# Kernel tuning notes

Hardware: AMD Instinct MI355X
Metric: run time of the kernel (lower is better)

The kernel has to match this reference:

```python
import jax, jax.numpy as jnp
import numpy as np

L, N, I, H = 512, 64, 1024, 1024


def setup_inputs() -> dict:
    key = jax.random.key(0)
    ks = jax.random.split(key, 7)
    s = 0.05
    return {
        "x": jax.random.normal(ks[0], (L, N, I), dtype=jnp.float32),
        "h0": jnp.zeros((N, H), dtype=jnp.float32),
        "c0": jnp.zeros((N, H), dtype=jnp.float32),
        "W_ih": jax.random.normal(ks[1], (4 * H, I), dtype=jnp.float32) * s,
        "W_hh": jax.random.normal(ks[2], (4 * H, H), dtype=jnp.float32) * s,
        "b_ih": jax.random.normal(ks[3], (4 * H,), dtype=jnp.float32) * s,
        "b_hh": jax.random.normal(ks[4], (4 * H,), dtype=jnp.float32) * s,
        "W_out": jax.random.normal(ks[5], (I, H), dtype=jnp.float32) * s,
        "b_out": jax.random.normal(ks[6], (I,), dtype=jnp.float32) * s,
    }


def reference(x, h0, c0, W_ih, W_hh, b_ih, b_hh, W_out, b_out):
    # PyTorch LSTMCell gate order: input, forget, cell(g), output
    b = b_ih + b_hh  # fuse the two bias adds

    def step(carry, xt):
        h, c = carry
        z = xt @ W_ih.T + h @ W_hh.T + b  # [N, 4H]
        i, f, g, o = jnp.split(z, 4, axis=1)
        c = jax.nn.sigmoid(f) * c + jax.nn.sigmoid(i) * jnp.tanh(g)
        h = jax.nn.sigmoid(o) * jnp.tanh(c)
        return (h, c), None

    (h, c), _ = jax.lax.scan(step, (h0, c0), x)
    y = h @ W_out.T + b_out  # [N, I]
    return (y, h, c)
```

## Files before the change

### kernel.cpp

```cpp
#include <hip/hip_runtime.h>
#include <hip/hip_bf16.h>


#define L_STEPS 512
#define NB 64
#define HID 1024
#define GRID_LSTM 128

typedef __bf16 bf16x8 __attribute__((ext_vector_type(8)));
typedef __bf16 bf16x4 __attribute__((ext_vector_type(4)));
typedef __bf16 bf16x2 __attribute__((ext_vector_type(2)));
typedef float  f32x4  __attribute__((ext_vector_type(4)));
typedef float  f32x2  __attribute__((ext_vector_type(2)));
typedef unsigned u32x4 __attribute__((ext_vector_type(4)));

__device__ __forceinline__ float sigmoid_f(float x) {
    return 1.f / (1.f + __expf(-x));
}
__device__ __forceinline__ float tanh_f(float x) {
    return 1.f - 2.f / (1.f + __expf(2.f * x));
}

__global__ void convert_kernel(const float* __restrict__ x, const float* __restrict__ h0,
                               __bf16* __restrict__ xbf, __bf16* __restrict__ hbf,
                               unsigned* __restrict__ bar) {
    unsigned u = blockIdx.x * 256u + threadIdx.x;
    if (u < 512u) bar[u] = 0u;
    const int row = u & 63;
    const int cg  = (u >> 6) & 127;
    if (u < 8192u) {
        const float* s = h0 + (size_t)row * HID + cg * 8;
        f32x4 a = *(const f32x4*)s, b = *(const f32x4*)(s + 4);
        bf16x8 o;
        o[0]=(__bf16)a[0]; o[1]=(__bf16)a[1]; o[2]=(__bf16)a[2]; o[3]=(__bf16)a[3];
        o[4]=(__bf16)b[0]; o[5]=(__bf16)b[1]; o[6]=(__bf16)b[2]; o[7]=(__bf16)b[3];
        ((bf16x8*)hbf)[u] = o;
    }
    const int t = u >> 13;
    const float* s = x + ((size_t)t * NB + row) * HID + cg * 8;
    f32x4 a = *(const f32x4*)s, b = *(const f32x4*)(s + 4);
    bf16x8 o;
    o[0]=(__bf16)a[0]; o[1]=(__bf16)a[1]; o[2]=(__bf16)a[2]; o[3]=(__bf16)a[3];
    o[4]=(__bf16)b[0]; o[5]=(__bf16)b[1]; o[6]=(__bf16)b[2]; o[7]=(__bf16)b[3];
    ((bf16x8*)xbf)[u] = o;
}

__device__ __forceinline__ void mfma_x(const __bf16* __restrict__ act,
                                       const bf16x8 (&wfr)[2][8],
                                       f32x4 (&acc)[2][4]) {
    #pragma unroll
    for (int kk = 0; kk < 8; ++kk) {
        bf16x8 bfr[4];
        #pragma unroll
        for (int nt = 0; nt < 4; ++nt)
            bfr[nt] = *(const bf16x8*)(act + kk * 2048 + nt * 128);
        #pragma unroll
        for (int mt = 0; mt < 2; ++mt)
            #pragma unroll
            for (int nt = 0; nt < 4; ++nt)
                acc[mt][nt] = __builtin_amdgcn_mfma_f32_16x16x32_bf16(
                    wfr[mt][kk], bfr[nt], acc[mt][nt], 0, 0, 0);
    }
}

template <bool RING>
__global__ __launch_bounds__(256, 1) void lstm_kernel(
    const float* __restrict__ c0,
    const float* __restrict__ W_ih, const float* __restrict__ W_hh,
    const float* __restrict__ b_ih, const float* __restrict__ b_hh,
    const __bf16* __restrict__ xbf,
    __bf16* hbuf,
    unsigned* bar,
    float* __restrict__ out)
{
    const int tid  = threadIdx.x;
    const int lane = tid & 63;
    const int w    = tid >> 6;
    const int quad = lane >> 4;
    const int l15  = lane & 15;
    const int hbase = blockIdx.x * 8;

    __shared__ float red[4][64][44];

    bf16x8 wfx[2][8], wfh[2][8];
    #pragma unroll
    for (int mt = 0; mt < 2; ++mt) {
        const int n    = mt * 16 + l15;
        const int grow = (n >> 3) * HID + hbase + (n & 7);
        #pragma unroll
        for (int kk = 0; kk < 8; ++kk) {
            const int kcol = w * 256 + kk * 32 + quad * 8;
            {
                const float* src = W_ih + (size_t)grow * 1024 + kcol;
                f32x4 a = *(const f32x4*)src;
                f32x4 b = *(const f32x4*)(src + 4);
                bf16x8 f;
                f[0]=(__bf16)a[0]; f[1]=(__bf16)a[1]; f[2]=(__bf16)a[2]; f[3]=(__bf16)a[3];
                f[4]=(__bf16)b[0]; f[5]=(__bf16)b[1]; f[6]=(__bf16)b[2]; f[7]=(__bf16)b[3];
                wfx[mt][kk] = f;
            }
            {
                const float* src = W_hh + (size_t)grow * 1024 + kcol;
                f32x4 a = *(const f32x4*)src;
                f32x4 b = *(const f32x4*)(src + 4);
                bf16x8 f;
                f[0]=(__bf16)a[0]; f[1]=(__bf16)a[1]; f[2]=(__bf16)a[2]; f[3]=(__bf16)a[3];
                f[4]=(__bf16)b[0]; f[5]=(__bf16)b[1]; f[6]=(__bf16)b[2]; f[7]=(__bf16)b[3];
                wfh[mt][kk] = f;
            }
        }
    }

    const int p0 = tid * 2;
    const int cb = p0 >> 3;
    const int cu = p0 & 7;
    float c0v = c0[cb * HID + hbase + cu];
    float c1v = c0[cb * HID + hbase + cu + 1];

    float bias0[4], bias1[4];
    #pragma unroll
    for (int gate = 0; gate < 4; ++gate) {
        int gr = gate * HID + hbase + cu;
        bias0[gate] = b_ih[gr] + b_hh[gr];
        bias1[gate] = b_ih[gr + 1] + b_hh[gr + 1];
    }

    const int lane_off = (32 * w + quad) * 512 + l15 * 8;
    const int hstore_off = blockIdx.x * 512 + cb * 8 + cu;

    f32x4 acc[2][4];
    #pragma unroll
    for (int mt = 0; mt < 2; ++mt)
        #pragma unroll
        for (int nt = 0; nt < 4; ++nt) { f32x4 z = {0.f,0.f,0.f,0.f}; acc[mt][nt] = z; }
    mfma_x(xbf + lane_off, wfx, acc);

    const int pf0 = 128 * w + lane;
    const int pf1 = 128 * w + 64 + lane;

    for (int t = 0; t < L_STEPS; ++t) {
        for (;;) {
            unsigned f0 = __hip_atomic_load(&bar[pf0], __ATOMIC_RELAXED,
                                            __HIP_MEMORY_SCOPE_AGENT);
            unsigned f1 = __hip_atomic_load(&bar[pf1], __ATOMIC_RELAXED,
                                            __HIP_MEMORY_SCOPE_AGENT);
            if (__all((f0 >= (unsigned)t) && (f1 >= (unsigned)t))) break;
            __builtin_amdgcn_s_sleep(1);
        }

        u32x4 hb[8][4];
        const __bf16* hb_base = hbuf
            + (size_t)(RING ? t : (t & 1)) * (NB * HID) + lane_off;
        #pragma unroll
        for (int kk = 0; kk < 8; ++kk)
            #pragma unroll
            for (int nt = 0; nt < 4; ++nt) {
                const __bf16* p = hb_base + kk * 2048 + nt * 128;
                if constexpr (RING)
                    asm volatile("global_load_dwordx4 %0, %1, off"
                                 : "=v"(hb[kk][nt]) : "v"(p));
                else
                    asm volatile("global_load_dwordx4 %0, %1, off sc1"
                                 : "=v"(hb[kk][nt]) : "v"(p));
            }
        asm volatile("s_waitcnt vmcnt(16)"
            : "+v"(hb[0][0]), "+v"(hb[0][1]), "+v"(hb[0][2]), "+v"(hb[0][3]),
              "+v"(hb[1][0]), "+v"(hb[1][1]), "+v"(hb[1][2]), "+v"(hb[1][3]),
              "+v"(hb[2][0]), "+v"(hb[2][1]), "+v"(hb[2][2]), "+v"(hb[2][3]),
              "+v"(hb[3][0]), "+v"(hb[3][1]), "+v"(hb[3][2]), "+v"(hb[3][3]));
        #pragma unroll
        for (int kk = 0; kk < 4; ++kk)
            #pragma unroll
            for (int mt = 0; mt < 2; ++mt)
                #pragma unroll
                for (int nt = 0; nt < 4; ++nt)
                    acc[mt][nt] = __builtin_amdgcn_mfma_f32_16x16x32_bf16(
                        wfh[mt][kk], __builtin_bit_cast(bf16x8, hb[kk][nt]),
                        acc[mt][nt], 0, 0, 0);
        asm volatile("s_waitcnt vmcnt(0)"
            : "+v"(hb[4][0]), "+v"(hb[4][1]), "+v"(hb[4][2]), "+v"(hb[4][3]),
              "+v"(hb[5][0]), "+v"(hb[5][1]), "+v"(hb[5][2]), "+v"(hb[5][3]),
              "+v"(hb[6][0]), "+v"(hb[6][1]), "+v"(hb[6][2]), "+v"(hb[6][3]),
              "+v"(hb[7][0]), "+v"(hb[7][1]), "+v"(hb[7][2]), "+v"(hb[7][3]));
        #pragma unroll
        for (int kk = 4; kk < 8; ++kk)
            #pragma unroll
            for (int mt = 0; mt < 2; ++mt)
                #pragma unroll
                for (int nt = 0; nt < 4; ++nt)
                    acc[mt][nt] = __builtin_amdgcn_mfma_f32_16x16x32_bf16(
                        wfh[mt][kk], __builtin_bit_cast(bf16x8, hb[kk][nt]),
                        acc[mt][nt], 0, 0, 0);

        __syncthreads();

        #pragma unroll
        for (int mt = 0; mt < 2; ++mt)
            #pragma unroll
            for (int nt = 0; nt < 4; ++nt) {
                const int row0 = mt * 16 + quad * 4;
                const int col  = nt * 16 + l15;
                *(f32x4*)&red[w][col][row0] = acc[mt][nt];
            }
        __syncthreads();

        float h0v, h1v;
        {
            float z0[4], z1[4];
            #pragma unroll
            for (int gate = 0; gate < 4; ++gate) {
                const int row = gate * 8 + cu;
                f32x2 s0 = *(const f32x2*)&red[0][cb][row];
                f32x2 s1 = *(const f32x2*)&red[1][cb][row];
                f32x2 s2 = *(const f32x2*)&red[2][cb][row];
                f32x2 s3 = *(const f32x2*)&red[3][cb][row];
                z0[gate] = s0[0] + s1[0] + s2[0] + s3[0] + bias0[gate];
                z1[gate] = s0[1] + s1[1] + s2[1] + s3[1] + bias1[gate];
            }
            float ig = sigmoid_f(z0[0]), fg = sigmoid_f(z0[1]);
            float gg = tanh_f(z0[2]),    og = sigmoid_f(z0[3]);
            c0v = fg * c0v + ig * gg;
            h0v = og * tanh_f(c0v);
            ig = sigmoid_f(z1[0]); fg = sigmoid_f(z1[1]);
            gg = tanh_f(z1[2]);    og = sigmoid_f(z1[3]);
            c1v = fg * c1v + ig * gg;
            h1v = og * tanh_f(c1v);
        }

        {
            bf16x2 hv; hv[0] = (__bf16)h0v; hv[1] = (__bf16)h1v;
            unsigned hbits = __builtin_bit_cast(unsigned, hv);
            const __bf16* dst = hbuf
                + (size_t)(RING ? (t + 1) : ((t + 1) & 1)) * (NB * HID) + hstore_off;
            asm volatile("global_store_dword %0, %1, off sc1"
                         :: "v"(dst), "v"(hbits) : "memory");
        }
        if (t == L_STEPS - 1) {
            const int idx = cb * HID + hbase + cu;
            out[65536 + idx]      = h0v;
            out[65536 + idx + 1]  = h1v;
            out[131072 + idx]     = c0v;
            out[131072 + idx + 1] = c1v;
        }
        asm volatile("s_waitcnt vmcnt(0)" ::: "memory");
        if (lane == 0)
            __hip_atomic_store(&bar[blockIdx.x * 4 + w], (unsigned)(t + 1),
                               __ATOMIC_RELAXED, __HIP_MEMORY_SCOPE_AGENT);

        #pragma unroll
        for (int mt = 0; mt < 2; ++mt)
            #pragma unroll
            for (int nt = 0; nt < 4; ++nt) { f32x4 z = {0.f,0.f,0.f,0.f}; acc[mt][nt] = z; }
        if (t < L_STEPS - 1)
            mfma_x(xbf + (size_t)(t + 1) * (NB * HID) + lane_off, wfx, acc);
    }
}

__global__ void out_kernel(const float* __restrict__ base, const float* __restrict__ Wout,
                           const float* __restrict__ bout, float* __restrict__ y)
{
    const int wv   = (int)((blockIdx.x * 256u + threadIdx.x) >> 6);
    const int lane = threadIdx.x & 63;
    const int b = wv >> 10;
    const int i = wv & 1023;
    const f32x4* hp = (const f32x4*)(base + 65536 + b * HID);
    const f32x4* wp = (const f32x4*)(Wout + (size_t)i * HID);
    float acc = 0.f;
    #pragma unroll
    for (int q = 0; q < 4; ++q) {
        f32x4 hv = hp[q * 64 + lane];
        f32x4 wvv = wp[q * 64 + lane];
        acc += hv[0]*wvv[0] + hv[1]*wvv[1] + hv[2]*wvv[2] + hv[3]*wvv[3];
    }
    #pragma unroll
    for (int off = 32; off > 0; off >>= 1) acc += __shfl_down(acc, off);
    if (lane == 0) y[b * HID + i] = acc + bout[i];
}

extern "C" void kernel_launch(void* const* d_in, const int* in_sizes, int n_in,
                              void* d_out, int out_size, void* d_ws, size_t ws_size,
                              hipStream_t stream)
{
    const float* x    = (const float*)d_in[0];
    const float* h0   = (const float*)d_in[1];
    const float* c0   = (const float*)d_in[2];
    const float* W_ih = (const float*)d_in[3];
    const float* W_hh = (const float*)d_in[4];
    const float* b_ih = (const float*)d_in[5];
    const float* b_hh = (const float*)d_in[6];
    const float* Wout = (const float*)d_in[7];
    const float* bout = (const float*)d_in[8];
    float* out = (float*)d_out;

    const size_t XBF_B  = 67108864;
    const size_t RING_B = 513ull * 131072;
    const size_t need_ring = XBF_B + RING_B + 2048;
    const bool ring = ws_size >= need_ring;

    char* ws = (char*)d_ws;
    __bf16* xbf   = (__bf16*)(ws);
    __bf16* hbuf  = (__bf16*)(ws + XBF_B);
    unsigned* bar = (unsigned*)(ws + XBF_B + (ring ? RING_B : 262144));

    convert_kernel<<<16384, 256, 0, stream>>>(x, h0, xbf, hbuf, bar);
    if (ring)
        lstm_kernel<true><<<GRID_LSTM, 256, 0, stream>>>(c0, W_ih, W_hh, b_ih, b_hh,
                                                         xbf, hbuf, bar, out);
    else
        lstm_kernel<false><<<GRID_LSTM, 256, 0, stream>>>(c0, W_ih, W_hh, b_ih, b_hh,
                                                          xbf, hbuf, bar, out);
    out_kernel<<<16384, 256, 0, stream>>>(out, Wout, bout, out);
}
```

Measured before the change: 2.917 ms.

## Pipeline the LSTM step across four batch groups with per-group readiness flags

The 64-wide batch is split into four 16-column groups, each with its own readiness flag. Every block now waits only for that group's h slice, runs its recurrent MFMAs, reduces through shared memory, and one wave does the gate math and publishes that group's h. The next step's input-projection MFMAs for a group are issued before its flag is signalled. The aim is to replace the coarse whole-step spin barrier with fine-grained dataflow, so consumers can start on early groups while later ones are still in flight. In exchange there are four times as many flag polls and __syncthreads per step, and the gate math is serialized onto one wave per group.

```diff
diff --git a/kernel.cpp b/kernel.cpp
--- a/kernel.cpp
+++ b/kernel.cpp
@@ -45,21 +45,15 @@
     ((bf16x8*)xbf)[u] = o;
 }
 
-__device__ __forceinline__ void mfma_x(const __bf16* __restrict__ act,
-                                       const bf16x8 (&wfr)[2][8],
-                                       f32x4 (&acc)[2][4]) {
+__device__ __forceinline__ void mfma_x_bg(const __bf16* __restrict__ act,
+                                          const bf16x8 (&wfr)[2][8],
+                                          f32x4 (&a)[2]) {
     #pragma unroll
     for (int kk = 0; kk < 8; ++kk) {
-        bf16x8 bfr[4];
-        #pragma unroll
-        for (int nt = 0; nt < 4; ++nt)
-            bfr[nt] = *(const bf16x8*)(act + kk * 2048 + nt * 128);
+        bf16x8 b = *(const bf16x8*)(act + kk * 2048);
         #pragma unroll
         for (int mt = 0; mt < 2; ++mt)
-            #pragma unroll
-            for (int nt = 0; nt < 4; ++nt)
-                acc[mt][nt] = __builtin_amdgcn_mfma_f32_16x16x32_bf16(
-                    wfr[mt][kk], bfr[nt], acc[mt][nt], 0, 0, 0);
+            a[mt] = __builtin_amdgcn_mfma_f32_16x16x32_bf16(wfr[mt][kk], b, a[mt], 0, 0, 0);
     }
 }
 
@@ -128,131 +122,111 @@
     const int lane_off = (32 * w + quad) * 512 + l15 * 8;
     const int hstore_off = blockIdx.x * 512 + cb * 8 + cu;
 
-    f32x4 acc[2][4];
-    #pragma unroll
-    for (int mt = 0; mt < 2; ++mt)
-        #pragma unroll
-        for (int nt = 0; nt < 4; ++nt) { f32x4 z = {0.f,0.f,0.f,0.f}; acc[mt][nt] = z; }
-    mfma_x(xbf + lane_off, wfx, acc);
-
-    const int pf0 = 128 * w + lane;
-    const int pf1 = 128 * w + 64 + lane;
+    const int pfl = (32 * w + (lane & 31)) * 4;
+
+    f32x4 acc[4][2];
+    #pragma unroll
+    for (int bg = 0; bg < 4; ++bg) {
+        #pragma unroll
+        for (int mt = 0; mt < 2; ++mt) { f32x4 z = {0.f,0.f,0.f,0.f}; acc[bg][mt] = z; }
+        mfma_x_bg(xbf + lane_off + bg * 128, wfx, acc[bg]);
+    }
 
     for (int t = 0; t < L_STEPS; ++t) {
-        for (;;) {
-            unsigned f0 = __hip_atomic_load(&bar[pf0], __ATOMIC_RELAXED,
-                                            __HIP_MEMORY_SCOPE_AGENT);
-            unsigned f1 = __hip_atomic_load(&bar[pf1], __ATOMIC_RELAXED,
-                                            __HIP_MEMORY_SCOPE_AGENT);
-            if (__all((f0 >= (unsigned)t) && (f1 >= (unsigned)t))) break;
-            __builtin_amdgcn_s_sleep(1);
-        }
-
-        u32x4 hb[8][4];
-        const __bf16* hb_base = hbuf
-            + (size_t)(RING ? t : (t & 1)) * (NB * HID) + lane_off;
-        #pragma unroll
-        for (int kk = 0; kk < 8; ++kk)
-            #pragma unroll
-            for (int nt = 0; nt < 4; ++nt) {
-                const __bf16* p = hb_base + kk * 2048 + nt * 128;
+        const __bf16* hb_slot = hbuf + (size_t)(RING ? t : (t & 1)) * (NB * HID) + lane_off;
+        #pragma unroll
+        for (int bg = 0; bg < 4; ++bg) {
+            for (;;) {
+                unsigned f = __hip_atomic_load(&bar[pfl + bg], __ATOMIC_RELAXED,
+                                               __HIP_MEMORY_SCOPE_AGENT);
+                if (__all(f >= (unsigned)t)) break;
+                __builtin_amdgcn_s_sleep(1);
+            }
+
+            u32x4 hb[8];
+            #pragma unroll
+            for (int kk = 0; kk < 8; ++kk) {
+                const __bf16* p = hb_slot + bg * 128 + kk * 2048;
                 if constexpr (RING)
                     asm volatile("global_load_dwordx4 %0, %1, off"
-                                 : "=v"(hb[kk][nt]) : "v"(p));
+                                 : "=v"(hb[kk]) : "v"(p));
                 else
                     asm volatile("global_load_dwordx4 %0, %1, off sc1"
-                                 : "=v"(hb[kk][nt]) : "v"(p));
-            }
-        asm volatile("s_waitcnt vmcnt(16)"
-            : "+v"(hb[0][0]), "+v"(hb[0][1]), "+v"(hb[0][2]), "+v"(hb[0][3]),
-              "+v"(hb[1][0]), "+v"(hb[1][1]), "+v"(hb[1][2]), "+v"(hb[1][3]),
-              "+v"(hb[2][0]), "+v"(hb[2][1]), "+v"(hb[2][2]), "+v"(hb[2][3]),
-              "+v"(hb[3][0]), "+v"(hb[3][1]), "+v"(hb[3][2]), "+v"(hb[3][3]));
-        #pragma unroll
-        for (int kk = 0; kk < 4; ++kk)
+                                 : "=v"(hb[kk]) : "v"(p));
+            }
+            asm volatile("s_waitcnt vmcnt(4)"
+                : "+v"(hb[0]), "+v"(hb[1]), "+v"(hb[2]), "+v"(hb[3]));
+            #pragma unroll
+            for (int kk = 0; kk < 4; ++kk)
+                #pragma unroll
+                for (int mt = 0; mt < 2; ++mt)
+                    acc[bg][mt] = __builtin_amdgcn_mfma_f32_16x16x32_bf16(
+                        wfh[mt][kk], __builtin_bit_cast(bf16x8, hb[kk]),
+                        acc[bg][mt], 0, 0, 0);
+            asm volatile("s_waitcnt vmcnt(0)"
+                : "+v"(hb[4]), "+v"(hb[5]), "+v"(hb[6]), "+v"(hb[7]));
+            #pragma unroll
+            for (int kk = 4; kk < 8; ++kk)
+                #pragma unroll
+                for (int mt = 0; mt < 2; ++mt)
+                    acc[bg][mt] = __builtin_amdgcn_mfma_f32_16x16x32_bf16(
+                        wfh[mt][kk], __builtin_bit_cast(bf16x8, hb[kk]),
+                        acc[bg][mt], 0, 0, 0);
+
             #pragma unroll
             for (int mt = 0; mt < 2; ++mt)
-                #pragma unroll
-                for (int nt = 0; nt < 4; ++nt)
-                    acc[mt][nt] = __builtin_amdgcn_mfma_f32_16x16x32_bf16(
-                        wfh[mt][kk], __builtin_bit_cast(bf16x8, hb[kk][nt]),
-                        acc[mt][nt], 0, 0, 0);
-        asm volatile("s_waitcnt vmcnt(0)"
-            : "+v"(hb[4][0]), "+v"(hb[4][1]), "+v"(hb[4][2]), "+v"(hb[4][3]),
-              "+v"(hb[5][0]), "+v"(hb[5][1]), "+v"(hb[5][2]), "+v"(hb[5][3]),
-              "+v"(hb[6][0]), "+v"(hb[6][1]), "+v"(hb[6][2]), "+v"(hb[6][3]),
-              "+v"(hb[7][0]), "+v"(hb[7][1]), "+v"(hb[7][2]), "+v"(hb[7][3]));
-        #pragma unroll
-        for (int kk = 4; kk < 8; ++kk)
-            #pragma unroll
-            for (int mt = 0; mt < 2; ++mt)
-                #pragma unroll
-                for (int nt = 0; nt < 4; ++nt)
-                    acc[mt][nt] = __builtin_amdgcn_mfma_f32_16x16x32_bf16(
-                        wfh[mt][kk], __builtin_bit_cast(bf16x8, hb[kk][nt]),
-                        acc[mt][nt], 0, 0, 0);
-
-        __syncthreads();
-
-        #pragma unroll
-        for (int mt = 0; mt < 2; ++mt)
-            #pragma unroll
-            for (int nt = 0; nt < 4; ++nt) {
-                const int row0 = mt * 16 + quad * 4;
-                const int col  = nt * 16 + l15;
-                *(f32x4*)&red[w][col][row0] = acc[mt][nt];
-            }
-        __syncthreads();
-
-        float h0v, h1v;
-        {
-            float z0[4], z1[4];
-            #pragma unroll
-            for (int gate = 0; gate < 4; ++gate) {
-                const int row = gate * 8 + cu;
-                f32x2 s0 = *(const f32x2*)&red[0][cb][row];
-                f32x2 s1 = *(const f32x2*)&red[1][cb][row];
-                f32x2 s2 = *(const f32x2*)&red[2][cb][row];
-                f32x2 s3 = *(const f32x2*)&red[3][cb][row];
-                z0[gate] = s0[0] + s1[0] + s2[0] + s3[0] + bias0[gate];
-                z1[gate] = s0[1] + s1[1] + s2[1] + s3[1] + bias1[gate];
-            }
-            float ig = sigmoid_f(z0[0]), fg = sigmoid_f(z0[1]);
-            float gg = tanh_f(z0[2]),    og = sigmoid_f(z0[3]);
-            c0v = fg * c0v + ig * gg;
-            h0v = og * tanh_f(c0v);
-            ig = sigmoid_f(z1[0]); fg = sigmoid_f(z1[1]);
-            gg = tanh_f(z1[2]);    og = sigmoid_f(z1[3]);
-            c1v = fg * c1v + ig * gg;
-            h1v = og * tanh_f(c1v);
+                *(f32x4*)&red[w][bg * 16 + l15][mt * 16 + quad * 4] = acc[bg][mt];
+            __syncthreads();
+
+            if (w == bg) {
+                float z0[4], z1[4];
+                #pragma unroll
+                for (int gate = 0; gate < 4; ++gate) {
+                    const int row = gate * 8 + cu;
+                    f32x2 s0 = *(const f32x2*)&red[0][cb][row];
+                    f32x2 s1 = *(const f32x2*)&red[1][cb][row];
+                    f32x2 s2 = *(const f32x2*)&red[2][cb][row];
+                    f32x2 s3 = *(const f32x2*)&red[3][cb][row];
+                    z0[gate] = s0[0] + s1[0] + s2[0] + s3[0] + bias0[gate];
+                    z1[gate] = s0[1] + s1[1] + s2[1] + s3[1] + bias1[gate];
+                }
+                float ig = sigmoid_f(z0[0]), fg = sigmoid_f(z0[1]);
+                float gg = tanh_f(z0[2]),    og = sigmoid_f(z0[3]);
+                c0v = fg * c0v + ig * gg;
+                float h0v = og * tanh_f(c0v);
+                ig = sigmoid_f(z1[0]); fg = sigmoid_f(z1[1]);
+                gg = tanh_f(z1[2]);    og = sigmoid_f(z1[3]);
+                c1v = fg * c1v + ig * gg;
+                float h1v = og * tanh_f(c1v);
+
+                bf16x2 hv; hv[0] = (__bf16)h0v; hv[1] = (__bf16)h1v;
+                unsigned hbits = __builtin_bit_cast(unsigned, hv);
+                const __bf16* dst = hbuf
+                    + (size_t)(RING ? (t + 1) : ((t + 1) & 1)) * (NB * HID) + hstore_off;
+                asm volatile("global_store_dword %0, %1, off sc1"
+                             :: "v"(dst), "v"(hbits) : "memory");
+                if (t == L_STEPS - 1) {
+                    const int idx = cb * HID + hbase + cu;
+                    out[65536 + idx]      = h0v;
+                    out[65536 + idx + 1]  = h1v;
+                    out[131072 + idx]     = c0v;
+                    out[131072 + idx + 1] = c1v;
+                }
+            }
+
+            if (t < L_STEPS - 1) {
+                #pragma unroll
+                for (int mt = 0; mt < 2; ++mt) { f32x4 z = {0.f,0.f,0.f,0.f}; acc[bg][mt] = z; }
+                mfma_x_bg(xbf + (size_t)(t + 1) * (NB * HID) + lane_off + bg * 128,
+                          wfx, acc[bg]);
+                if (w == bg) {
+                    asm volatile("s_waitcnt vmcnt(0)" ::: "memory");
+                    if (lane == 0)
+                        __hip_atomic_store(&bar[blockIdx.x * 4 + bg], (unsigned)(t + 1),
+                                           __ATOMIC_RELAXED, __HIP_MEMORY_SCOPE_AGENT);
+                }
+            }
         }
-
-        {
-            bf16x2 hv; hv[0] = (__bf16)h0v; hv[1] = (__bf16)h1v;
-            unsigned hbits = __builtin_bit_cast(unsigned, hv);
-            const __bf16* dst = hbuf
-                + (size_t)(RING ? (t + 1) : ((t + 1) & 1)) * (NB * HID) + hstore_off;
-            asm volatile("global_store_dword %0, %1, off sc1"
-                         :: "v"(dst), "v"(hbits) : "memory");
-        }
-        if (t == L_STEPS - 1) {
-            const int idx = cb * HID + hbase + cu;
-            out[65536 + idx]      = h0v;
-            out[65536 + idx + 1]  = h1v;
-            out[131072 + idx]     = c0v;
-            out[131072 + idx + 1] = c1v;
-        }
-        asm volatile("s_waitcnt vmcnt(0)" ::: "memory");
-        if (lane == 0)
-            __hip_atomic_store(&bar[blockIdx.x * 4 + w], (unsigned)(t + 1),
-                               __ATOMIC_RELAXED, __HIP_MEMORY_SCOPE_AGENT);
-
-        #pragma unroll
-        for (int mt = 0; mt < 2; ++mt)
-            #pragma unroll
-            for (int nt = 0; nt < 4; ++nt) { f32x4 z = {0.f,0.f,0.f,0.f}; acc[mt][nt] = z; }
-        if (t < L_STEPS - 1)
-            mfma_x(xbf + (size_t)(t + 1) * (NB * HID) + lane_off, wfx, acc);
     }
 }
 
```

Result: slower. 5.567 ms (+90.9%).

## Precompute input projection in separate kernel and slim recurrent LSTM loop

Applied to the files above, without the earlier changes.

Adds a zx_kernel that computes x·W_ih^T plus the fused biases for all timesteps up front, stored in fp32 in a gate-interleaved layout. A new persistent lstm_wave kernel then only performs the h·W_hh^T MFMA per step, with W_hh held in registers. It uses per-producer flag polling instead of a global barrier, and reuses the consumed xbf slots to hold the bf16 hidden state. This takes the input projection off the serial critical path, at the cost of a 512MB workspace and extra memory traffic. If the workspace is too small it falls back to the old path.

```diff
diff --git a/kernel.cpp b/kernel.cpp
--- a/kernel.cpp
+++ b/kernel.cpp
@@ -5,10 +5,8 @@
 #define L_STEPS 512
 #define NB 64
 #define HID 1024
-#define GRID_LSTM 128
 
 typedef __bf16 bf16x8 __attribute__((ext_vector_type(8)));
-typedef __bf16 bf16x4 __attribute__((ext_vector_type(4)));
 typedef __bf16 bf16x2 __attribute__((ext_vector_type(2)));
 typedef float  f32x4  __attribute__((ext_vector_type(4)));
 typedef float  f32x2  __attribute__((ext_vector_type(2)));
@@ -25,7 +23,7 @@
                                __bf16* __restrict__ xbf, __bf16* __restrict__ hbf,
                                unsigned* __restrict__ bar) {
     unsigned u = blockIdx.x * 256u + threadIdx.x;
-    if (u < 512u) bar[u] = 0u;
+    if (u < 1024u) bar[u] = 0u;
     const int row = u & 63;
     const int cg  = (u >> 6) & 127;
     if (u < 8192u) {
@@ -43,6 +41,226 @@
     o[0]=(__bf16)a[0]; o[1]=(__bf16)a[1]; o[2]=(__bf16)a[2]; o[3]=(__bf16)a[3];
     o[4]=(__bf16)b[0]; o[5]=(__bf16)b[1]; o[6]=(__bf16)b[2]; o[7]=(__bf16)b[3];
     ((bf16x8*)xbf)[u] = o;
+}
+
+__global__ __launch_bounds__(256, 1) void zx_kernel(
+    const __bf16* __restrict__ xbf, const float* __restrict__ W_ih,
+    const float* __restrict__ b_ih, const float* __restrict__ b_hh,
+    float* __restrict__ zx)
+{
+    const int tid = threadIdx.x, lane = tid & 63, w = tid >> 6;
+    const int quad = lane >> 4, l15 = lane & 15;
+    const int cg = blockIdx.x >> 2, tq = blockIdx.x & 3;
+    const int hb16 = cg * 16;
+
+    __shared__ float red[4][64][66];
+
+    bf16x8 wfx[4][8];
+    #pragma unroll
+    for (int mt = 0; mt < 4; ++mt) {
+        const int grow = mt * HID + hb16 + l15;
+        #pragma unroll
+        for (int kk = 0; kk < 8; ++kk) {
+            const float* src = W_ih + (size_t)grow * HID + w * 256 + kk * 32 + quad * 8;
+            f32x4 a = *(const f32x4*)src, b = *(const f32x4*)(src + 4);
+            bf16x8 f;
+            f[0]=(__bf16)a[0]; f[1]=(__bf16)a[1]; f[2]=(__bf16)a[2]; f[3]=(__bf16)a[3];
+            f[4]=(__bf16)b[0]; f[5]=(__bf16)b[1]; f[6]=(__bf16)b[2]; f[7]=(__bf16)b[3];
+            wfx[mt][kk] = f;
+        }
+    }
+
+    const int co = tid >> 4;
+    const int b0 = (tid & 15) * 4;
+    float bias[4];
+    #pragma unroll
+    for (int g = 0; g < 4; ++g)
+        bias[g] = b_ih[g * HID + hb16 + co] + b_hh[g * HID + hb16 + co];
+
+    const int lane_off = (32 * w + quad) * 512 + l15 * 8;
+
+    for (int t = tq * 128; t < tq * 128 + 128; ++t) {
+        const __bf16* act = xbf + (size_t)t * 65536 + lane_off;
+        f32x4 acc[4][4];
+        #pragma unroll
+        for (int mt = 0; mt < 4; ++mt)
+            #pragma unroll
+            for (int nt = 0; nt < 4; ++nt) { f32x4 z = {0.f,0.f,0.f,0.f}; acc[mt][nt] = z; }
+        #pragma unroll
+        for (int kk = 0; kk < 8; ++kk) {
+            bf16x8 bfr[4];
+            #pragma unroll
+            for (int nt = 0; nt < 4; ++nt)
+                bfr[nt] = *(const bf16x8*)(act + kk * 2048 + nt * 128);
+            #pragma unroll
+            for (int mt = 0; mt < 4; ++mt)
+                #pragma unroll
+                for (int nt = 0; nt < 4; ++nt)
+                    acc[mt][nt] = __builtin_amdgcn_mfma_f32_16x16x32_bf16(
+                        wfx[mt][kk], bfr[nt], acc[mt][nt], 0, 0, 0);
+        }
+        __syncthreads();
+        #pragma unroll
+        for (int mt = 0; mt < 4; ++mt)
+            #pragma unroll
+            for (int nt = 0; nt < 4; ++nt)
+                *(f32x4*)&red[w][nt * 16 + l15][mt * 16 + quad * 4] = acc[mt][nt];
+        __syncthreads();
+        float* zrow = zx + (((size_t)t * HID + hb16 + co) * 64 + b0) * 4;
+        #pragma unroll
+        for (int j = 0; j < 4; ++j) {
+            const int b = b0 + j;
+            f32x4 zv;
+            #pragma unroll
+            for (int g = 0; g < 4; ++g)
+                zv[g] = bias[g] + red[0][b][g*16+co] + red[1][b][g*16+co]
+                                + red[2][b][g*16+co] + red[3][b][g*16+co];
+            *(f32x4*)(zrow + j * 4) = zv;
+        }
+    }
+}
+
+__global__ __launch_bounds__(512, 1) void lstm_wave(
+    const float* __restrict__ c0_p,
+    const float* __restrict__ W_hh,
+    __bf16* xbf,
+    const __bf16* __restrict__ h0s,
+    const float* __restrict__ zx,
+    unsigned* bar,
+    float* __restrict__ out)
+{
+    const int tid  = threadIdx.x;
+    const int lane = tid & 63;
+    const int w8   = tid >> 6;
+    const int nh   = w8 & 3;
+    const int mt   = w8 >> 2;
+    const int quad = lane >> 4;
+    const int l15  = lane & 15;
+    const int wg   = blockIdx.x;
+    const int hbase = wg * 8;
+
+    const int col   = hbase + mt * 4 + quad;
+    const int batch = nh * 16 + l15;
+
+    bf16x8 wfh[32];
+    {
+        const int wrow = (l15 & 3) * HID + hbase + mt * 4 + (l15 >> 2);
+        const float* wr = W_hh + (size_t)wrow * HID + quad * 8;
+        #pragma unroll
+        for (int kk = 0; kk < 32; ++kk) {
+            const float* src = wr + kk * 32;
+            f32x4 a = *(const f32x4*)src, b = *(const f32x4*)(src + 4);
+            bf16x8 f;
+            f[0]=(__bf16)a[0]; f[1]=(__bf16)a[1]; f[2]=(__bf16)a[2]; f[3]=(__bf16)a[3];
+            f[4]=(__bf16)b[0]; f[5]=(__bf16)b[1]; f[6]=(__bf16)b[2]; f[7]=(__bf16)b[3];
+            wfh[kk] = f;
+        }
+    }
+
+    float cv = c0_p[batch * HID + col];
+
+    const int bOff  = quad * 512 + nh * 128 + l15 * 8;
+    const int hsOff = wg * 512 + batch * 8 + (mt * 4 + quad);
+    const size_t zOff = ((size_t)col * 64 + batch) * 4;
+    const int fpost = nh * 256 + mt * 128 + wg;
+    const int pbase = nh * 256 + lane;
+
+    u32x4 zxr = *(const u32x4*)(zx + zOff);
+
+    for (int t = 0; t < L_STEPS; ++t) {
+        for (;;) {
+            unsigned f0 = __hip_atomic_load(&bar[pbase],       __ATOMIC_RELAXED, __HIP_MEMORY_SCOPE_AGENT);
+            unsigned f1 = __hip_atomic_load(&bar[pbase + 64],  __ATOMIC_RELAXED, __HIP_MEMORY_SCOPE_AGENT);
+            unsigned f2 = __hip_atomic_load(&bar[pbase + 128], __ATOMIC_RELAXED, __HIP_MEMORY_SCOPE_AGENT);
+            unsigned f3 = __hip_atomic_load(&bar[pbase + 192], __ATOMIC_RELAXED, __HIP_MEMORY_SCOPE_AGENT);
+            if (__all((f0 >= (unsigned)t) && (f1 >= (unsigned)t) &&
+                      (f2 >= (unsigned)t) && (f3 >= (unsigned)t))) break;
+            __builtin_amdgcn_s_sleep(1);
+        }
+
+        f32x4 acc_a = __builtin_bit_cast(f32x4, zxr);
+        f32x4 acc_b = {0.f, 0.f, 0.f, 0.f};
+
+        const __bf16* bp = ((t == 0) ? h0s : (const __bf16*)(xbf + (size_t)t * 65536)) + bOff;
+
+        u32x4 hb[16];
+        #pragma unroll
+        for (int k = 0; k < 16; ++k)
+            asm volatile("global_load_dwordx4 %0, %1, off" : "=v"(hb[k]) : "v"(bp + k * 2048));
+
+        asm volatile("s_waitcnt vmcnt(8)"
+            : "+v"(hb[0]), "+v"(hb[1]), "+v"(hb[2]), "+v"(hb[3]),
+              "+v"(hb[4]), "+v"(hb[5]), "+v"(hb[6]), "+v"(hb[7]));
+        #pragma unroll
+        for (int k = 0; k < 8; ++k) {
+            if (k & 1) acc_b = __builtin_amdgcn_mfma_f32_16x16x32_bf16(
+                wfh[k], __builtin_bit_cast(bf16x8, hb[k]), acc_b, 0, 0, 0);
+            else       acc_a = __builtin_amdgcn_mfma_f32_16x16x32_bf16(
+                wfh[k], __builtin_bit_cast(bf16x8, hb[k]), acc_a, 0, 0, 0);
+        }
+        #pragma unroll
+        for (int k = 0; k < 8; ++k)
+            asm volatile("global_load_dwordx4 %0, %1, off" : "=v"(hb[k]) : "v"(bp + (16 + k) * 2048));
+
+        asm volatile("s_waitcnt vmcnt(8)"
+            : "+v"(hb[8]), "+v"(hb[9]), "+v"(hb[10]), "+v"(hb[11]),
+              "+v"(hb[12]), "+v"(hb[13]), "+v"(hb[14]), "+v"(hb[15]));
+        #pragma unroll
+        for (int k = 8; k < 16; ++k) {
+            if (k & 1) acc_b = __builtin_amdgcn_mfma_f32_16x16x32_bf16(
+                wfh[k], __builtin_bit_cast(bf16x8, hb[k]), acc_b, 0, 0, 0);
+            else       acc_a = __builtin_amdgcn_mfma_f32_16x16x32_bf16(
+                wfh[k], __builtin_bit_cast(bf16x8, hb[k]), acc_a, 0, 0, 0);
+        }
+        #pragma unroll
+        for (int k = 0; k < 8; ++k)
+            asm volatile("global_load_dwordx4 %0, %1, off" : "=v"(hb[8 + k]) : "v"(bp + (24 + k) * 2048));
+
+        asm volatile("s_waitcnt vmcnt(8)"
+            : "+v"(hb[0]), "+v"(hb[1]), "+v"(hb[2]), "+v"(hb[3]),
+              "+v"(hb[4]), "+v"(hb[5]), "+v"(hb[6]), "+v"(hb[7]));
+        #pragma unroll
+        for (int k = 16; k < 24; ++k) {
+            if (k & 1) acc_b = __builtin_amdgcn_mfma_f32_16x16x32_bf16(
+                wfh[k], __builtin_bit_cast(bf16x8, hb[k - 16]), acc_b, 0, 0, 0);
+            else       acc_a = __builtin_amdgcn_mfma_f32_16x16x32_bf16(
+                wfh[k], __builtin_bit_cast(bf16x8, hb[k - 16]), acc_a, 0, 0, 0);
+        }
+        asm volatile("s_waitcnt vmcnt(0)"
+            : "+v"(hb[8]), "+v"(hb[9]), "+v"(hb[10]), "+v"(hb[11]),
+              "+v"(hb[12]), "+v"(hb[13]), "+v"(hb[14]), "+v"(hb[15]));
+        #pragma unroll
+        for (int k = 24; k < 32; ++k) {
+            if (k & 1) acc_b = __builtin_amdgcn_mfma_f32_16x16x32_bf16(
+                wfh[k], __builtin_bit_cast(bf16x8, hb[k - 16]), acc_b, 0, 0, 0);
+            else       acc_a = __builtin_amdgcn_mfma_f32_16x16x32_bf16(
+                wfh[k], __builtin_bit_cast(bf16x8, hb[k - 16]), acc_a, 0, 0, 0);
+        }
+
+        f32x4 z = acc_a + acc_b;
+        float ig = sigmoid_f(z[0]), fg = sigmoid_f(z[1]);
+        float gg = tanh_f(z[2]),    og = sigmoid_f(z[3]);
+        cv = fg * cv + ig * gg;
+        float hv = og * tanh_f(cv);
+
+        if (t < L_STEPS - 1) {
+            __bf16 hbf16 = (__bf16)hv;
+            unsigned hbits = (unsigned)__builtin_bit_cast(unsigned short, hbf16);
+            const __bf16* dst = xbf + (size_t)(t + 1) * 65536 + hsOff;
+            asm volatile("global_store_short %0, %1, off sc1"
+                         :: "v"(dst), "v"(hbits) : "memory");
+            const float* zp = zx + ((size_t)(t + 1) << 18) + zOff;
+            asm volatile("global_load_dwordx4 %0, %1, off" : "=v"(zxr) : "v"(zp));
+            asm volatile("s_waitcnt vmcnt(1)" ::: "memory");
+            if (lane == 0)
+                __hip_atomic_store(&bar[fpost], (unsigned)(t + 1),
+                                   __ATOMIC_RELAXED, __HIP_MEMORY_SCOPE_AGENT);
+        } else {
+            const int idx = batch * HID + col;
+            out[65536 + idx]  = hv;
+            out[131072 + idx] = cv;
+        }
+    }
 }
 
 __device__ __forceinline__ void mfma_x(const __bf16* __restrict__ act,
@@ -291,23 +509,40 @@
     const float* Wout = (const float*)d_in[7];
     const float* bout = (const float*)d_in[8];
     float* out = (float*)d_out;
-
-    const size_t XBF_B  = 67108864;
+    char* ws = (char*)d_ws;
+
+    const size_t XBF_B = 67108864ull;
+    const size_t H0_B  = 131072ull;
+    const size_t ZX_B  = 536870912ull;
+    const size_t BAR_B = 4096ull;
+    const size_t need_new = XBF_B + H0_B + ZX_B + BAR_B;
+
+    if (ws_size >= need_new) {
+        __bf16*   xbf = (__bf16*)ws;
+        __bf16*   h0s = (__bf16*)(ws + XBF_B);
+        float*    zxb = (float*)(ws + XBF_B + H0_B);
+        unsigned* bar = (unsigned*)(ws + XBF_B + H0_B + ZX_B);
+        convert_kernel<<<16384, 256, 0, stream>>>(x, h0, xbf, h0s, bar);
+        zx_kernel<<<256, 256, 0, stream>>>(xbf, W_ih, b_ih, b_hh, zxb);
+        lstm_wave<<<128, 512, 0, stream>>>(c0, W_hh, xbf, h0s, zxb, bar, out);
+        out_kernel<<<16384, 256, 0, stream>>>(out, Wout, bout, out);
+        return;
+    }
+
     const size_t RING_B = 513ull * 131072;
-    const size_t need_ring = XBF_B + RING_B + 2048;
+    const size_t need_ring = XBF_B + RING_B + 4096;
     const bool ring = ws_size >= need_ring;
 
-    char* ws = (char*)d_ws;
     __bf16* xbf   = (__bf16*)(ws);
     __bf16* hbuf  = (__bf16*)(ws + XBF_B);
     unsigned* bar = (unsigned*)(ws + XBF_B + (ring ? RING_B : 262144));
 
     convert_kernel<<<16384, 256, 0, stream>>>(x, h0, xbf, hbuf, bar);
     if (ring)
-        lstm_kernel<true><<<GRID_LSTM, 256, 0, stream>>>(c0, W_ih, W_hh, b_ih, b_hh,
-                                                         xbf, hbuf, bar, out);
+        lstm_kernel<true><<<128, 256, 0, stream>>>(c0, W_ih, W_hh, b_ih, b_hh,
+                                                   xbf, hbuf, bar, out);
     else
-        lstm_kernel<false><<<GRID_LSTM, 256, 0, stream>>>(c0, W_ih, W_hh, b_ih, b_hh,
-                                                          xbf, hbuf, bar, out);
+        lstm_kernel<false><<<128, 256, 0, stream>>>(c0, W_ih, W_hh, b_ih, b_hh,
+                                                    xbf, hbuf, bar, out);
     out_kernel<<<16384, 256, 0, stream>>>(out, Wout, bout, out);
 }
```

Result: no change. 2.926 ms (+0.3%).

## Replace LSTM grid barrier with canary-based per-slot data-ready polling

Applied to the files above, without the earlier changes.

Adds a new persistent LSTM kernel that drops the global atomic barrier between timesteps. Readiness is detected by polling for a NaN-like canary value written into the next hidden-state ring slots two steps ahead. Hidden-state loads go through inline asm in two halves, with a fallback re-poll for any fragment still holding the canary, so the recurrent MFMAs can start as soon as the data arrives. The risk is that it relies on ordering and visibility of relaxed stores, and on a real bf16 pair never equalling the canary bit pattern.

```diff
diff --git a/kernel.cpp b/kernel.cpp
--- a/kernel.cpp
+++ b/kernel.cpp
@@ -6,9 +6,9 @@
 #define NB 64
 #define HID 1024
 #define GRID_LSTM 128
+#define CANARY 0x7FC17FC1u
 
 typedef __bf16 bf16x8 __attribute__((ext_vector_type(8)));
-typedef __bf16 bf16x4 __attribute__((ext_vector_type(4)));
 typedef __bf16 bf16x2 __attribute__((ext_vector_type(2)));
 typedef float  f32x4  __attribute__((ext_vector_type(4)));
 typedef float  f32x2  __attribute__((ext_vector_type(2)));
@@ -25,7 +25,8 @@
                                __bf16* __restrict__ xbf, __bf16* __restrict__ hbf,
                                unsigned* __restrict__ bar) {
     unsigned u = blockIdx.x * 256u + threadIdx.x;
-    if (u < 512u) bar[u] = 0u;
+    if (u < 1024u) bar[u] = 0u;
+    if (u < 32768u) ((unsigned*)hbf)[32768u + u] = CANARY;
     const int row = u & 63;
     const int cg  = (u >> 6) & 127;
     if (u < 8192u) {
@@ -60,6 +61,236 @@
             for (int nt = 0; nt < 4; ++nt)
                 acc[mt][nt] = __builtin_amdgcn_mfma_f32_16x16x32_bf16(
                     wfr[mt][kk], bfr[nt], acc[mt][nt], 0, 0, 0);
+    }
+}
+
+__device__ __forceinline__ bool frag_bad(const u32x4& v) {
+    return (v[0] == CANARY) | (v[1] == CANARY) | (v[2] == CANARY) | (v[3] == CANARY);
+}
+__device__ __forceinline__ void fix_frag(u32x4& v, __bf16* p) {
+    unsigned* dp = (unsigned*)p;
+    while (__any(frag_bad(v))) {
+        v[0] = __hip_atomic_load(dp + 0, __ATOMIC_RELAXED, __HIP_MEMORY_SCOPE_AGENT);
+        v[1] = __hip_atomic_load(dp + 1, __ATOMIC_RELAXED, __HIP_MEMORY_SCOPE_AGENT);
+        v[2] = __hip_atomic_load(dp + 2, __ATOMIC_RELAXED, __HIP_MEMORY_SCOPE_AGENT);
+        v[3] = __hip_atomic_load(dp + 3, __ATOMIC_RELAXED, __HIP_MEMORY_SCOPE_AGENT);
+    }
+}
+
+__global__ __launch_bounds__(256, 1) void lstm_canary(
+    const float* __restrict__ c0,
+    const float* __restrict__ W_ih, const float* __restrict__ W_hh,
+    const float* __restrict__ b_ih, const float* __restrict__ b_hh,
+    const __bf16* __restrict__ xbf,
+    __bf16* hbuf,
+    float* __restrict__ out)
+{
+    const int tid  = threadIdx.x;
+    const int lane = tid & 63;
+    const int w    = tid >> 6;
+    const int quad = lane >> 4;
+    const int l15  = lane & 15;
+    const int wg   = blockIdx.x;
+    const int hbase = wg * 8;
+
+    __shared__ float red[4][64][44];
+
+    bf16x8 wfx[2][8], wfh[2][8];
+    #pragma unroll
+    for (int mt = 0; mt < 2; ++mt) {
+        const int n    = mt * 16 + l15;
+        const int grow = (n >> 3) * HID + hbase + (n & 7);
+        #pragma unroll
+        for (int kk = 0; kk < 8; ++kk) {
+            const int kcol = w * 256 + kk * 32 + quad * 8;
+            {
+                const float* src = W_ih + (size_t)grow * 1024 + kcol;
+                f32x4 a = *(const f32x4*)src;
+                f32x4 b = *(const f32x4*)(src + 4);
+                bf16x8 f;
+                f[0]=(__bf16)a[0]; f[1]=(__bf16)a[1]; f[2]=(__bf16)a[2]; f[3]=(__bf16)a[3];
+                f[4]=(__bf16)b[0]; f[5]=(__bf16)b[1]; f[6]=(__bf16)b[2]; f[7]=(__bf16)b[3];
+                wfx[mt][kk] = f;
+            }
+            {
+                const float* src = W_hh + (size_t)grow * 1024 + kcol;
+                f32x4 a = *(const f32x4*)src;
+                f32x4 b = *(const f32x4*)(src + 4);
+                bf16x8 f;
+                f[0]=(__bf16)a[0]; f[1]=(__bf16)a[1]; f[2]=(__bf16)a[2]; f[3]=(__bf16)a[3];
+                f[4]=(__bf16)b[0]; f[5]=(__bf16)b[1]; f[6]=(__bf16)b[2]; f[7]=(__bf16)b[3];
+                wfh[mt][kk] = f;
+            }
+        }
+    }
+
+    const int p0 = tid * 2;
+    const int cb = p0 >> 3;
+    const int cu = p0 & 7;
+    float c0v = c0[cb * HID + hbase + cu];
+    float c1v = c0[cb * HID + hbase + cu + 1];
+
+    float bias0[4], bias1[4];
+    #pragma unroll
+    for (int gate = 0; gate < 4; ++gate) {
+        int gr = gate * HID + hbase + cu;
+        bias0[gate] = b_ih[gr] + b_hh[gr];
+        bias1[gate] = b_ih[gr + 1] + b_hh[gr + 1];
+    }
+
+    const int lane_off = (32 * w + quad) * 512 + l15 * 8;
+    const int hstore_off = wg * 512 + cb * 8 + cu;
+    unsigned* pfp_base = (unsigned*)hbuf + wg * 256 + tid;
+    const unsigned pO = (unsigned)(32 * w + (lane >> 1)) * 256u
+                      + (unsigned)((lane & 1) * 4) * 32u;
+
+    f32x4 acc[2][4];
+    #pragma unroll
+    for (int mt = 0; mt < 2; ++mt)
+        #pragma unroll
+        for (int nt = 0; nt < 4; ++nt) { f32x4 z = {0.f,0.f,0.f,0.f}; acc[mt][nt] = z; }
+    mfma_x(xbf + lane_off, wfx, acc);
+
+    for (int t = 0; t < L_STEPS; ++t) {
+        if (t <= L_STEPS - 3)
+            __hip_atomic_store(pfp_base + (size_t)(t + 2) * 32768, CANARY,
+                               __ATOMIC_RELAXED, __HIP_MEMORY_SCOPE_AGENT);
+
+        {
+            unsigned* sd = (unsigned*)hbuf + (size_t)t * 32768 + pO;
+            for (;;) {
+                unsigned a = __hip_atomic_load(sd +  0, __ATOMIC_RELAXED, __HIP_MEMORY_SCOPE_AGENT);
+                unsigned b = __hip_atomic_load(sd + 32, __ATOMIC_RELAXED, __HIP_MEMORY_SCOPE_AGENT);
+                unsigned c = __hip_atomic_load(sd + 64, __ATOMIC_RELAXED, __HIP_MEMORY_SCOPE_AGENT);
+                unsigned d = __hip_atomic_load(sd + 96, __ATOMIC_RELAXED, __HIP_MEMORY_SCOPE_AGENT);
+                if (__all((a != CANARY) && (b != CANARY) &&
+                          (c != CANARY) && (d != CANARY))) break;
+            }
+        }
+
+        u32x4 hb[8][4];
+        __bf16* hb_base = hbuf + (size_t)t * (NB * HID) + lane_off;
+        #pragma unroll
+        for (int kk = 0; kk < 8; ++kk)
+            #pragma unroll
+            for (int nt = 0; nt < 4; ++nt) {
+                const __bf16* p = hb_base + kk * 2048 + nt * 128;
+                asm volatile("global_load_dwordx4 %0, %1, off"
+                             : "=v"(hb[kk][nt]) : "v"(p));
+            }
+        asm volatile("s_waitcnt vmcnt(16)"
+            : "+v"(hb[0][0]), "+v"(hb[0][1]), "+v"(hb[0][2]), "+v"(hb[0][3]),
+              "+v"(hb[1][0]), "+v"(hb[1][1]), "+v"(hb[1][2]), "+v"(hb[1][3]),
+              "+v"(hb[2][0]), "+v"(hb[2][1]), "+v"(hb[2][2]), "+v"(hb[2][3]),
+              "+v"(hb[3][0]), "+v"(hb[3][1]), "+v"(hb[3][2]), "+v"(hb[3][3]));
+        {
+            bool anyb = false;
+            #pragma unroll
+            for (int kk = 0; kk < 4; ++kk)
+                #pragma unroll
+                for (int nt = 0; nt < 4; ++nt) anyb |= frag_bad(hb[kk][nt]);
+            if (__builtin_expect(__any(anyb), 0)) {
+                #pragma unroll
+                for (int kk = 0; kk < 4; ++kk)
+                    #pragma unroll
+                    for (int nt = 0; nt < 4; ++nt)
+                        fix_frag(hb[kk][nt], hb_base + kk * 2048 + nt * 128);
+            }
+        }
+        #pragma unroll
+        for (int kk = 0; kk < 4; ++kk)
+            #pragma unroll
+            for (int mt = 0; mt < 2; ++mt)
+                #pragma unroll
+                for (int nt = 0; nt < 4; ++nt)
+                    acc[mt][nt] = __builtin_amdgcn_mfma_f32_16x16x32_bf16(
+                        wfh[mt][kk], __builtin_bit_cast(bf16x8, hb[kk][nt]),
+                        acc[mt][nt], 0, 0, 0);
+        asm volatile("s_waitcnt vmcnt(0)"
+            : "+v"(hb[4][0]), "+v"(hb[4][1]), "+v"(hb[4][2]), "+v"(hb[4][3]),
+              "+v"(hb[5][0]), "+v"(hb[5][1]), "+v"(hb[5][2]), "+v"(hb[5][3]),
+              "+v"(hb[6][0]), "+v"(hb[6][1]), "+v"(hb[6][2]), "+v"(hb[6][3]),
+              "+v"(hb[7][0]), "+v"(hb[7][1]), "+v"(hb[7][2]), "+v"(hb[7][3]));
+        {
+            bool anyb = false;
+            #pragma unroll
+            for (int kk = 4; kk < 8; ++kk)
+                #pragma unroll
+                for (int nt = 0; nt < 4; ++nt) anyb |= frag_bad(hb[kk][nt]);
+            if (__builtin_expect(__any(anyb), 0)) {
+                #pragma unroll
+                for (int kk = 4; kk < 8; ++kk)
+                    #pragma unroll
+                    for (int nt = 0; nt < 4; ++nt)
+                        fix_frag(hb[kk][nt], hb_base + kk * 2048 + nt * 128);
+            }
+        }
+        #pragma unroll
+        for (int kk = 4; kk < 8; ++kk)
+            #pragma unroll
+            for (int mt = 0; mt < 2; ++mt)
+                #pragma unroll
+                for (int nt = 0; nt < 4; ++nt)
+                    acc[mt][nt] = __builtin_amdgcn_mfma_f32_16x16x32_bf16(
+                        wfh[mt][kk], __builtin_bit_cast(bf16x8, hb[kk][nt]),
+                        acc[mt][nt], 0, 0, 0);
+
+        __syncthreads();
+
+        #pragma unroll
+        for (int mt = 0; mt < 2; ++mt)
+            #pragma unroll
+            for (int nt = 0; nt < 4; ++nt) {
+                const int row0 = mt * 16 + quad * 4;
+                const int col  = nt * 16 + l15;
+                *(f32x4*)&red[w][col][row0] = acc[mt][nt];
+            }
+        __syncthreads();
+
+        float h0v, h1v;
+        {
+            float z0[4], z1[4];
+            #pragma unroll
+            for (int gate = 0; gate < 4; ++gate) {
+                const int row = gate * 8 + cu;
+                f32x2 s0 = *(const f32x2*)&red[0][cb][row];
+                f32x2 s1 = *(const f32x2*)&red[1][cb][row];
+                f32x2 s2 = *(const f32x2*)&red[2][cb][row];
+                f32x2 s3 = *(const f32x2*)&red[3][cb][row];
+                z0[gate] = s0[0] + s1[0] + s2[0] + s3[0] + bias0[gate];
+                z1[gate] = s0[1] + s1[1] + s2[1] + s3[1] + bias1[gate];
+            }
+            float ig = sigmoid_f(z0[0]), fg = sigmoid_f(z0[1]);
+            float gg = tanh_f(z0[2]),    og = sigmoid_f(z0[3]);
+            c0v = fg * c0v + ig * gg;
+            h0v = og * tanh_f(c0v);
+            ig = sigmoid_f(z1[0]); fg = sigmoid_f(z1[1]);
+            gg = tanh_f(z1[2]);    og = sigmoid_f(z1[3]);
+            c1v = fg * c1v + ig * gg;
+            h1v = og * tanh_f(c1v);
+        }
+
+        {
+            bf16x2 hv; hv[0] = (__bf16)h0v; hv[1] = (__bf16)h1v;
+            unsigned hbits = __builtin_bit_cast(unsigned, hv);
+            const __bf16* dst = hbuf + (size_t)(t + 1) * (NB * HID) + hstore_off;
+            asm volatile("global_store_dword %0, %1, off sc1"
+                         :: "v"(dst), "v"(hbits) : "memory");
+        }
+        if (t == L_STEPS - 1) {
+            const int idx = cb * HID + hbase + cu;
+            out[65536 + idx]      = h0v;
+            out[65536 + idx + 1]  = h1v;
+            out[131072 + idx]     = c0v;
+            out[131072 + idx + 1] = c1v;
+        }
+
+        #pragma unroll
+        for (int mt = 0; mt < 2; ++mt)
+            #pragma unroll
+            for (int nt = 0; nt < 4; ++nt) { f32x4 z = {0.f,0.f,0.f,0.f}; acc[mt][nt] = z; }
+        if (t < L_STEPS - 1)
+            mfma_x(xbf + (size_t)(t + 1) * (NB * HID) + lane_off, wfx, acc);
     }
 }
 
@@ -291,21 +522,21 @@
     const float* Wout = (const float*)d_in[7];
     const float* bout = (const float*)d_in[8];
     float* out = (float*)d_out;
+    char* ws = (char*)d_ws;
 
     const size_t XBF_B  = 67108864;
     const size_t RING_B = 513ull * 131072;
-    const size_t need_ring = XBF_B + RING_B + 2048;
+    const size_t need_ring = XBF_B + RING_B + 4096;
     const bool ring = ws_size >= need_ring;
 
-    char* ws = (char*)d_ws;
     __bf16* xbf   = (__bf16*)(ws);
     __bf16* hbuf  = (__bf16*)(ws + XBF_B);
     unsigned* bar = (unsigned*)(ws + XBF_B + (ring ? RING_B : 262144));
 
     convert_kernel<<<16384, 256, 0, stream>>>(x, h0, xbf, hbuf, bar);
     if (ring)
-        lstm_kernel<true><<<GRID_LSTM, 256, 0, stream>>>(c0, W_ih, W_hh, b_ih, b_hh,
-                                                         xbf, hbuf, bar, out);
+        lstm_canary<<<GRID_LSTM, 256, 0, stream>>>(c0, W_ih, W_hh, b_ih, b_hh,
+                                                   xbf, hbuf, out);
     else
         lstm_kernel<false><<<GRID_LSTM, 256, 0, stream>>>(c0, W_ih, W_hh, b_ih, b_hh,
                                                           xbf, hbuf, bar, out);
```

Result: slower. 3.490 ms (+19.7%).
